# Performance work log

Measured on AMD Instinct MI355X. Metric: run time of the kernel, lower is better.

## Reference

```python
import jax, jax.numpy as jnp
import numpy as np
from jax import lax

EPS = 1e-6
MATCH_THRESHOLD = 0.3
N_DISCRETE_STEPS = 5
DT = 0.01
TWO_PI = 2.0 * np.pi


def setup_inputs() -> dict:
    key = jax.random.key(0)
    ks = jax.random.split(key, 6)
    N, M, D, H, n_osc = 8192, 8192, 4, 64, 28
    detections_t = jax.random.normal(ks[0], (N, D), dtype=jnp.float32)
    detections_t1 = jax.random.normal(ks[1], (M, D), dtype=jnp.float32)
    phase_W1 = jax.random.normal(ks[2], (D, H), dtype=jnp.float32) * (1.0 / np.sqrt(D))
    phase_b1 = jax.random.normal(ks[3], (H,), dtype=jnp.float32) * 0.05
    phase_W2 = jax.random.normal(ks[4], (H, n_osc), dtype=jnp.float32) * (1.0 / np.sqrt(H))
    phase_b2 = jax.random.normal(ks[5], (n_osc,), dtype=jnp.float32) * 0.05
    # fixed oscillator frequencies buffer: [2]*4 + [6]*8 + [40]*16
    frequencies = jnp.concatenate([
        jnp.full((4,), 2.0, jnp.float32),
        jnp.full((8,), 6.0, jnp.float32),
        jnp.full((16,), 40.0, jnp.float32),
    ])
    return {
        'detections_t': detections_t,
        'detections_t1': detections_t1,
        'phase_W1': phase_W1,
        'phase_b1': phase_b1,
        'phase_W2': phase_W2,
        'phase_b2': phase_b2,
        'frequencies': frequencies,
    }


def _encode_phase(x, W1, b1, W2, b2):
    h = jax.nn.relu(x @ W1 + b1)
    raw = h @ W2 + b2
    return raw % TWO_PI  # [N, n_osc]


def _similarity(phase_a, phase_b):
    # real(sum_k e^{i a_k} e^{-i b_k}) = cos(a)@cos(b).T + sin(a)@sin(b).T
    ca, sa = jnp.cos(phase_a), jnp.sin(phase_a)
    cb, sb = jnp.cos(phase_b), jnp.sin(phase_b)
    na = jnp.sqrt(jnp.sum(ca * ca + sa * sa, axis=-1, keepdims=True)) + EPS  # [N,1]
    nb = jnp.sqrt(jnp.sum(cb * cb + sb * sb, axis=-1, keepdims=True)) + EPS  # [M,1]
    sim = (ca @ cb.T + sa @ sb.T) / (na * nb.T)  # [N, M]
    return sim


def reference(detections_t, detections_t1, phase_W1, phase_b1, phase_W2, phase_b2, frequencies):
    phase_t = _encode_phase(detections_t, phase_W1, phase_b1, phase_W2, phase_b2)
    phase_t1 = _encode_phase(detections_t1, phase_W1, phase_b1, phase_W2, phase_b2)

    # uncoupled phase advance (n_discrete_steps fixed small loop)
    phase = phase_t
    for _ in range(N_DISCRETE_STEPS):
        phase = (phase + TWO_PI * frequencies * DT) % TWO_PI

    sim = _similarity(phase, phase_t1)  # [N, M]

    N = detections_t.shape[0]
    M = detections_t1.shape[0]
    max_sims = jnp.max(sim, axis=1)
    max_idxs = jnp.argmax(sim, axis=1)
    order = jnp.argsort(-max_sims)  # descending

    def body(i, carry):
        matches, used = carry
        idx = order[i]
        j = max_idxs[idx]
        ok = jnp.logical_and(jnp.logical_not(used[j]), max_sims[idx] > MATCH_THRESHOLD)
        matches = matches.at[idx].set(jnp.where(ok, j, -1))
        used = used.at[j].set(jnp.logical_or(used[j], ok))
        return (matches, used)

    matches0 = jnp.full((N,), -1, dtype=jnp.int32)
    used0 = jnp.zeros((M,), dtype=bool)
    matches, _ = lax.fori_loop(0, N, body, (matches0, used0))
    return (matches, sim)
```

## Files before the change

kernel.cpp:

```cpp
#include <hip/hip_runtime.h>
#include <math.h>

#define NR 8192
#define N_OSC 28
#define TWO_PI_F 6.28318530717958647692f
#define PLANE 524288

typedef __attribute__((ext_vector_type(8))) short s16x8;
typedef __attribute__((ext_vector_type(16))) float f32x16;
typedef __attribute__((ext_vector_type(4))) float f32x4;
typedef __attribute__((ext_vector_type(4))) unsigned int u32x4;

__device__ __forceinline__ float modpos(float x) {
    float r = fmodf(x, TWO_PI_F);
    if (r < 0.0f) r += TWO_PI_F;
    return r;
}
__device__ __forceinline__ unsigned fmono(float f) {
    unsigned u = __float_as_uint(f);
    return (u & 0x80000000u) ? ~u : (u | 0x80000000u);
}
__device__ __forceinline__ unsigned short f2bf(float f) {
    unsigned u = __float_as_uint(f);
    return (unsigned short)((u + 0x7FFFu + ((u >> 16) & 1u)) >> 16);
}
__device__ __forceinline__ float bf2f(unsigned short h) {
    return __uint_as_float(((unsigned)h) << 16);
}


__global__ __launch_bounds__(256, 1) void encode_kernel(
    const float* __restrict__ detA, const float* __restrict__ detB,
    const float* __restrict__ W1, const float* __restrict__ b1,
    const float* __restrict__ W2, const float* __restrict__ b2,
    const float* __restrict__ freq,
    unsigned short* __restrict__ tabA, unsigned short* __restrict__ tabB,
    float* __restrict__ normA, float* __restrict__ normB)
{
    __shared__ float sW1[4 * 64];
    __shared__ float sb1[64];
    __shared__ float sW2[64 * N_OSC];
    __shared__ float sb2[N_OSC];
    __shared__ float sDelta[N_OSC];

    int t = threadIdx.x;
    for (int i = t; i < 4 * 64; i += 256) sW1[i] = W1[i];
    for (int i = t; i < 64; i += 256) sb1[i] = b1[i];
    for (int i = t; i < 64 * N_OSC; i += 256) sW2[i] = W2[i];
    for (int i = t; i < N_OSC; i += 256) {
        sb2[i] = b2[i];
        sDelta[i] = (TWO_PI_F * freq[i]) * 0.01f;
    }
    __syncthreads();

    int gid = blockIdx.x * 256 + t;
    bool isA = gid < NR;
    int row = isA ? gid : gid - NR;
    const float* det = isA ? detA : detB;
    unsigned short* tab = isA ? tabA : tabB;
    float* nrm = isA ? normA : normB;

    float4 xv = *(const float4*)(det + (size_t)row * 4);
    float x0 = xv.x, x1 = xv.y, x2 = xv.z, x3 = xv.w;

    float h[64];
#pragma unroll
    for (int j = 0; j < 64; ++j) {
        float a = x0 * sW1[0 * 64 + j];
        a += x1 * sW1[1 * 64 + j];
        a += x2 * sW1[2 * 64 + j];
        a += x3 * sW1[3 * 64 + j];
        a += sb1[j];
        h[j] = fmaxf(a, 0.0f);
    }

    float raw[N_OSC];
#pragma unroll
    for (int o = 0; o < N_OSC; ++o) raw[o] = 0.0f;
#pragma unroll
    for (int j = 0; j < 64; ++j) {
        float hj = h[j];
#pragma unroll
        for (int o = 0; o < N_OSC; ++o) raw[o] += hj * sW2[j * N_OSC + o];
    }

    unsigned h2[32], m2[32], l2[32];
#pragma unroll
    for (int i = 0; i < 32; ++i) { h2[i] = 0u; m2[i] = 0u; l2[i] = 0u; }

    float csum = 0.0f;
#pragma unroll
    for (int o = 0; o < N_OSC; ++o) {
        float p = raw[o] + sb2[o];
        p = modpos(p);
        if (isA) {
            float d = sDelta[o];
#pragma unroll
            for (int s = 0; s < 5; ++s) { p = modpos(p + d); }
        }
        float sn, cs;
        sincosf(p, &sn, &cs);
        csum += cs * cs + sn * sn;
        {
            unsigned short v0 = f2bf(cs); float r1 = cs - bf2f(v0);
            unsigned short v1 = f2bf(r1); float r2 = r1 - bf2f(v1);
            unsigned short v2 = f2bf(r2);
            const int k = o, i = k >> 1, sh = (k & 1) * 16;
            h2[i] |= ((unsigned)v0) << sh;
            m2[i] |= ((unsigned)v1) << sh;
            l2[i] |= ((unsigned)v2) << sh;
        }
        {
            unsigned short v0 = f2bf(sn); float r1 = sn - bf2f(v0);
            unsigned short v1 = f2bf(r1); float r2 = r1 - bf2f(v1);
            unsigned short v2 = f2bf(r2);
            const int k = 28 + o, i = k >> 1, sh = (k & 1) * 16;
            h2[i] |= ((unsigned)v0) << sh;
            m2[i] |= ((unsigned)v1) << sh;
            l2[i] |= ((unsigned)v2) << sh;
        }
    }

    size_t gbase = (size_t)(row >> 5) * 2048 + (size_t)(row & 31) * 8;
#pragma unroll
    for (int c = 0; c < 8; ++c) {
        size_t off = gbase + (size_t)(c >> 1) * 512 + (size_t)(c & 1) * 256;
        u32x4 vh, vm, vl;
#pragma unroll
        for (int e = 0; e < 4; ++e) {
            vh[e] = h2[c * 4 + e]; vm[e] = m2[c * 4 + e]; vl[e] = l2[c * 4 + e];
        }
        *(u32x4*)(tab + off) = vh;
        *(u32x4*)(tab + PLANE + off) = vm;
        *(u32x4*)(tab + 2 * PLANE + off) = vl;
    }
    nrm[row] = 1.0f / (sqrtf(csum) + 1e-6f);
}

#define MFMA(a, b, c) __builtin_amdgcn_mfma_f32_32x32x16_bf16((a), (b), (c), 0, 0, 0)

__global__ __launch_bounds__(256) void sim_kernel(
    const unsigned short* __restrict__ tabA, const unsigned short* __restrict__ tabB,
    const float* __restrict__ normA, const float* __restrict__ normB,
    float* __restrict__ simOut, unsigned long long* __restrict__ rowMax)
{
    __shared__ __align__(16) float scrAll[4][64 * 68];

    int bid = blockIdx.x;
    int swz = (bid & 7) * 512 + (bid >> 3);
    int bx = swz & 63, by = swz >> 6;
    int r0 = by * 128, c0 = bx * 128;

    int t = threadIdx.x, w = t >> 6, l = t & 63;
    int wr = w >> 1, wc = w & 1;
    int lrow = l & 31;
    int gA = (r0 + wr * 64) >> 5;
    int gB = (c0 + wc * 64) >> 5;
    size_t l8 = (size_t)l * 8;

#define LD(tab, pl, g, ks) \
    (*(const s16x8*)((tab) + (size_t)(pl) * PLANE + (size_t)(g) * 2048 + (size_t)(ks) * 512 + l8))

    f32x16 acc00, acc01, acc10, acc11;
#pragma unroll
    for (int r = 0; r < 16; ++r) { acc00[r] = 0.f; acc01[r] = 0.f; acc10[r] = 0.f; acc11[r] = 0.f; }

#pragma unroll
    for (int ks = 0; ks < 4; ++ks) {
        s16x8 ah0 = LD(tabA, 0, gA, ks),     ah1 = LD(tabA, 0, gA + 1, ks);
        s16x8 bh0 = LD(tabB, 0, gB, ks),     bh1 = LD(tabB, 0, gB + 1, ks);
        s16x8 am0 = LD(tabA, 1, gA, ks),     am1 = LD(tabA, 1, gA + 1, ks);
        s16x8 bm0 = LD(tabB, 1, gB, ks),     bm1 = LD(tabB, 1, gB + 1, ks);
        s16x8 al0 = LD(tabA, 2, gA, ks),     al1 = LD(tabA, 2, gA + 1, ks);
        s16x8 bl0 = LD(tabB, 2, gB, ks),     bl1 = LD(tabB, 2, gB + 1, ks);

        acc00 = MFMA(ah0, bh0, acc00); acc01 = MFMA(ah0, bh1, acc01);
        acc10 = MFMA(ah1, bh0, acc10); acc11 = MFMA(ah1, bh1, acc11);
        acc00 = MFMA(ah0, bm0, acc00); acc01 = MFMA(ah0, bm1, acc01);
        acc10 = MFMA(ah1, bm0, acc10); acc11 = MFMA(ah1, bm1, acc11);
        acc00 = MFMA(am0, bh0, acc00); acc01 = MFMA(am0, bh1, acc01);
        acc10 = MFMA(am1, bh0, acc10); acc11 = MFMA(am1, bh1, acc11);
        acc00 = MFMA(am0, bm0, acc00); acc01 = MFMA(am0, bm1, acc01);
        acc10 = MFMA(am1, bm0, acc10); acc11 = MFMA(am1, bm1, acc11);
        acc00 = MFMA(ah0, bl0, acc00); acc01 = MFMA(ah0, bl1, acc01);
        acc10 = MFMA(ah1, bl0, acc10); acc11 = MFMA(ah1, bl1, acc11);
        acc00 = MFMA(al0, bh0, acc00); acc01 = MFMA(al0, bh1, acc01);
        acc10 = MFMA(al1, bh0, acc10); acc11 = MFMA(al1, bh1, acc11);
    }
#undef LD

    float icn0 = normB[c0 + wc * 64 + lrow];
    float icn1 = normB[c0 + wc * 64 + 32 + lrow];

    float* scr = scrAll[w];

#pragma unroll
    for (int r = 0; r < 16; ++r) {
        int rd0 = (r & 3) + 8 * (r >> 2) + 4 * (l >> 5);
        float irn0 = normA[r0 + wr * 64 + rd0];
        scr[rd0 * 68 + lrow]      = acc00[r] * (irn0 * icn0);
        scr[rd0 * 68 + 32 + lrow] = acc01[r] * (irn0 * icn1);
        int rd1 = rd0 + 32;
        float irn1 = normA[r0 + wr * 64 + rd1];
        scr[rd1 * 68 + lrow]      = acc10[r] * (irn1 * icn0);
        scr[rd1 * 68 + 32 + lrow] = acc11[r] * (irn1 * icn1);
    }

#pragma unroll
    for (int s = 0; s < 16; ++s) {
        int lr = 4 * s + (l >> 4);
        f32x4 v = *(const f32x4*)&scr[lr * 68 + (l & 15) * 4];
        int grow = r0 + wr * 64 + lr;
        __builtin_nontemporal_store(v,
            (f32x4*)&simOut[(size_t)grow * NR + c0 + wc * 64 + (l & 15) * 4]);
    }

    {
        const float* rp = &scr[l * 68];
        float mv = -2.0f; int mc = 0;
#pragma unroll
        for (int c4 = 0; c4 < 16; ++c4) {
            f32x4 v = *(const f32x4*)&rp[c4 * 4];
#pragma unroll
            for (int e = 0; e < 4; ++e) {
                bool g = v[e] > mv;
                mv = g ? v[e] : mv;
                mc = g ? c4 * 4 + e : mc;
            }
        }
        int grow = r0 + wr * 64 + l;
        unsigned gcol = (unsigned)(c0 + wc * 64 + mc);
        unsigned long long key = ((unsigned long long)fmono(mv) << 32)
                               | (unsigned long long)(0xFFFFFFFFu - gcol);
        atomicMax(&rowMax[grow], key);
    }
}

__global__ __launch_bounds__(256) void rowwin_kernel(
    const unsigned long long* __restrict__ rowMax,
    unsigned long long* __restrict__ colWin,
    float* __restrict__ outMatches)
{
    int r = blockIdx.x * 256 + threadIdx.x;
    if (r >= NR) return;
    outMatches[r] = -1.0f;
    unsigned long long key = rowMax[r];
    unsigned m = (unsigned)(key >> 32);
    unsigned bits = (m & 0x80000000u) ? (m ^ 0x80000000u) : ~m;
    float ms = __uint_as_float(bits);
    unsigned col = 0xFFFFFFFFu - (unsigned)key;
    if (ms > 0.3f) {
        unsigned long long ck = ((unsigned long long)m << 32)
                              | (unsigned long long)(0xFFFFFFFFu - (unsigned)r);
        atomicMax(&colWin[col], ck);
    }
}

__global__ __launch_bounds__(256) void colfin_kernel(
    const unsigned long long* __restrict__ colWin,
    float* __restrict__ outMatches)
{
    int j = blockIdx.x * 256 + threadIdx.x;
    if (j >= NR) return;
    unsigned long long w = colWin[j];
    if (w != 0ull) {
        unsigned r = 0xFFFFFFFFu - (unsigned)w;
        outMatches[r] = (float)j;
    }
}

extern "C" void kernel_launch(void* const* d_in, const int* in_sizes, int n_in,
                              void* d_out, int out_size, void* d_ws, size_t ws_size,
                              hipStream_t stream) {
    const float* detA = (const float*)d_in[0];
    const float* detB = (const float*)d_in[1];
    const float* W1   = (const float*)d_in[2];
    const float* b1   = (const float*)d_in[3];
    const float* W2   = (const float*)d_in[4];
    const float* b2   = (const float*)d_in[5];
    const float* freq = (const float*)d_in[6];
    float* out = (float*)d_out;

    char* ws = (char*)d_ws;
    unsigned short* tabA = (unsigned short*)(ws);
    unsigned short* tabB = (unsigned short*)(ws + 3145728);
    float* normA = (float*)(ws + 6291456);
    float* normB = (float*)(ws + 6324224);
    unsigned long long* rowMax = (unsigned long long*)(ws + 6356992);
    unsigned long long* colWin = (unsigned long long*)(ws + 6422528);

    (void)hipMemsetAsync(rowMax, 0, NR * 8, stream);
    (void)hipMemsetAsync(colWin, 0, NR * 8, stream);

    encode_kernel<<<64, 256, 0, stream>>>(detA, detB, W1, b1, W2, b2, freq,
                                          tabA, tabB, normA, normB);
    sim_kernel<<<4096, 256, 0, stream>>>(tabA, tabB, normA, normB, out + NR, rowMax);
    rowwin_kernel<<<NR / 256, 256, 0, stream>>>(rowMax, colWin, out);
    colfin_kernel<<<NR / 256, 256, 0, stream>>>(colWin, out);
}
```

Measured before the change: 150.3 us.

## Stage shared A tile in LDS via direct global-to-LDS loads, prefetch B into registers

Each block's A operand tile (three bf16 planes for 128 rows) is now loaded once into shared memory with global_load_lds and read by both column waves, instead of every wave fetching it from global memory. B fragments for all four k-steps are loaded into registers up front so their latency overlaps with the A staging. The LDS region is then reused as the per-wave epilogue scratch after a barrier, and launch bounds now request one block per CU. This adds barriers and raises register pressure, and the kernel is likely dominated by writing the large similarity output, so the gain may be small.

```diff
diff --git a/kernel.cpp b/kernel.cpp
--- a/kernel.cpp
+++ b/kernel.cpp
@@ -10,6 +10,9 @@
 typedef __attribute__((ext_vector_type(16))) float f32x16;
 typedef __attribute__((ext_vector_type(4))) float f32x4;
 typedef __attribute__((ext_vector_type(4))) unsigned int u32x4;
+
+#define AS3(p) ((__attribute__((address_space(3))) void*)(p))
+#define AS1C(p) ((const __attribute__((address_space(1))) void*)(p))
 
 __device__ __forceinline__ float modpos(float x) {
     float r = fmodf(x, TWO_PI_F);
@@ -139,12 +142,13 @@
 
 #define MFMA(a, b, c) __builtin_amdgcn_mfma_f32_32x32x16_bf16((a), (b), (c), 0, 0, 0)
 
-__global__ __launch_bounds__(256) void sim_kernel(
+__global__ __launch_bounds__(256, 1) void sim_kernel(
     const unsigned short* __restrict__ tabA, const unsigned short* __restrict__ tabB,
     const float* __restrict__ normA, const float* __restrict__ normB,
     float* __restrict__ simOut, unsigned long long* __restrict__ rowMax)
 {
-    __shared__ __align__(16) float scrAll[4][64 * 68];
+    __shared__ __align__(16) unsigned char smem[69632];
+    unsigned short* Ash = (unsigned short*)smem;
 
     int bid = blockIdx.x;
     int swz = (bid & 7) * 512 + (bid >> 3);
@@ -154,45 +158,67 @@
     int t = threadIdx.x, w = t >> 6, l = t & 63;
     int wr = w >> 1, wc = w & 1;
     int lrow = l & 31;
-    int gA = (r0 + wr * 64) >> 5;
     int gB = (c0 + wc * 64) >> 5;
+    int gr0 = r0 >> 5;
     size_t l8 = (size_t)l * 8;
 
-#define LD(tab, pl, g, ks) \
+#define GLD(tab, pl, g, ks) \
     (*(const s16x8*)((tab) + (size_t)(pl) * PLANE + (size_t)(g) * 2048 + (size_t)(ks) * 512 + l8))
 
+    s16x8 bh0[4], bh1[4], bm0[4], bm1[4], bl0[4], bl1[4];
+#pragma unroll
+    for (int ks = 0; ks < 4; ++ks) {
+        bh0[ks] = GLD(tabB, 0, gB, ks);  bh1[ks] = GLD(tabB, 0, gB + 1, ks);
+        bm0[ks] = GLD(tabB, 1, gB, ks);  bm1[ks] = GLD(tabB, 1, gB + 1, ks);
+        bl0[ks] = GLD(tabB, 2, gB, ks);  bl1[ks] = GLD(tabB, 2, gB + 1, ks);
+    }
+#undef GLD
+
+#pragma unroll
+    for (int i = 0; i < 12; ++i) {
+        int unit = w * 12 + i;
+        int p = unit >> 4, rem = unit & 15;
+        int g = rem >> 2, ks = rem & 3;
+        const unsigned short* src = tabA + (size_t)p * PLANE
+            + (size_t)(gr0 + g) * 2048 + (size_t)ks * 512 + l8;
+        __builtin_amdgcn_global_load_lds(AS1C(src), AS3(Ash + unit * 512), 16, 0, 0);
+    }
+    __builtin_amdgcn_sched_barrier(0);
+    __syncthreads();
+
     f32x16 acc00, acc01, acc10, acc11;
 #pragma unroll
     for (int r = 0; r < 16; ++r) { acc00[r] = 0.f; acc01[r] = 0.f; acc10[r] = 0.f; acc11[r] = 0.f; }
 
+    const char* Ab = (const char*)Ash + (size_t)wr * 8192 + (size_t)l * 16;
+#define LDA(p, gg, ks) (*(const s16x8*)(Ab + ((p) * 16384 + (gg) * 4096 + (ks) * 1024)))
+
 #pragma unroll
     for (int ks = 0; ks < 4; ++ks) {
-        s16x8 ah0 = LD(tabA, 0, gA, ks),     ah1 = LD(tabA, 0, gA + 1, ks);
-        s16x8 bh0 = LD(tabB, 0, gB, ks),     bh1 = LD(tabB, 0, gB + 1, ks);
-        s16x8 am0 = LD(tabA, 1, gA, ks),     am1 = LD(tabA, 1, gA + 1, ks);
-        s16x8 bm0 = LD(tabB, 1, gB, ks),     bm1 = LD(tabB, 1, gB + 1, ks);
-        s16x8 al0 = LD(tabA, 2, gA, ks),     al1 = LD(tabA, 2, gA + 1, ks);
-        s16x8 bl0 = LD(tabB, 2, gB, ks),     bl1 = LD(tabB, 2, gB + 1, ks);
-
-        acc00 = MFMA(ah0, bh0, acc00); acc01 = MFMA(ah0, bh1, acc01);
-        acc10 = MFMA(ah1, bh0, acc10); acc11 = MFMA(ah1, bh1, acc11);
-        acc00 = MFMA(ah0, bm0, acc00); acc01 = MFMA(ah0, bm1, acc01);
-        acc10 = MFMA(ah1, bm0, acc10); acc11 = MFMA(ah1, bm1, acc11);
-        acc00 = MFMA(am0, bh0, acc00); acc01 = MFMA(am0, bh1, acc01);
-        acc10 = MFMA(am1, bh0, acc10); acc11 = MFMA(am1, bh1, acc11);
-        acc00 = MFMA(am0, bm0, acc00); acc01 = MFMA(am0, bm1, acc01);
-        acc10 = MFMA(am1, bm0, acc10); acc11 = MFMA(am1, bm1, acc11);
-        acc00 = MFMA(ah0, bl0, acc00); acc01 = MFMA(ah0, bl1, acc01);
-        acc10 = MFMA(ah1, bl0, acc10); acc11 = MFMA(ah1, bl1, acc11);
-        acc00 = MFMA(al0, bh0, acc00); acc01 = MFMA(al0, bh1, acc01);
-        acc10 = MFMA(al1, bh0, acc10); acc11 = MFMA(al1, bh1, acc11);
-    }
-#undef LD
+        s16x8 ah0 = LDA(0, 0, ks), ah1 = LDA(0, 1, ks);
+        s16x8 am0 = LDA(1, 0, ks), am1 = LDA(1, 1, ks);
+        s16x8 al0 = LDA(2, 0, ks), al1 = LDA(2, 1, ks);
+
+        acc00 = MFMA(ah0, bh0[ks], acc00); acc01 = MFMA(ah0, bh1[ks], acc01);
+        acc10 = MFMA(ah1, bh0[ks], acc10); acc11 = MFMA(ah1, bh1[ks], acc11);
+        acc00 = MFMA(ah0, bm0[ks], acc00); acc01 = MFMA(ah0, bm1[ks], acc01);
+        acc10 = MFMA(ah1, bm0[ks], acc10); acc11 = MFMA(ah1, bm1[ks], acc11);
+        acc00 = MFMA(am0, bh0[ks], acc00); acc01 = MFMA(am0, bh1[ks], acc01);
+        acc10 = MFMA(am1, bh0[ks], acc10); acc11 = MFMA(am1, bh1[ks], acc11);
+        acc00 = MFMA(am0, bm0[ks], acc00); acc01 = MFMA(am0, bm1[ks], acc01);
+        acc10 = MFMA(am1, bm0[ks], acc10); acc11 = MFMA(am1, bm1[ks], acc11);
+        acc00 = MFMA(ah0, bl0[ks], acc00); acc01 = MFMA(ah0, bl1[ks], acc01);
+        acc10 = MFMA(ah1, bl0[ks], acc10); acc11 = MFMA(ah1, bl1[ks], acc11);
+        acc00 = MFMA(al0, bh0[ks], acc00); acc01 = MFMA(al0, bh1[ks], acc01);
+        acc10 = MFMA(al1, bh0[ks], acc10); acc11 = MFMA(al1, bh1[ks], acc11);
+    }
+#undef LDA
 
     float icn0 = normB[c0 + wc * 64 + lrow];
     float icn1 = normB[c0 + wc * 64 + 32 + lrow];
 
-    float* scr = scrAll[w];
+    __syncthreads();
+    float* scr = (float*)(smem + w * 17408);
 
 #pragma unroll
     for (int r = 0; r < 16; ++r) {
```

New measurement: 149.4 us. Within noise of the previous version (-0.6%).
